# Kernel optimization log

Hardware: AMD Instinct MI355X
Metric: run time of the kernel (lower is better)

Reference implementation:

```python
import jax, jax.numpy as jnp
import numpy as np

B, T0, T, N, C, MS, K, I = 8, 12, 10, 3000, 64, 3, 3, 1
W = T - (MS - 1)           # 8 sliding windows / stack_gcn layers
K2 = MS + (MS - 1) * I     # conv2 kernel width = 5
DN = ('NCHW', 'OIHW', 'NCHW')


def setup_inputs() -> dict:
    key = jax.random.key(0)
    ks = jax.random.split(key, 11)
    s = 0.05
    return {
        'original_data': jax.random.normal(ks[0], (B, T0, N, C), jnp.float32),
        'data': jax.random.normal(ks[1], (B, T, N, C), jnp.float32),
        'adj_st': jax.random.uniform(ks[2], (N, MS * N), jnp.float32) * 0.01,
        'conv1_w': jax.random.normal(ks[3], (2 * C, C, 1, MS), jnp.float32) * s,
        'conv1_b': jax.random.normal(ks[4], (2 * C,), jnp.float32) * s,
        'conv2_w': jax.random.normal(ks[5], (2 * C, C, 1, K2), jnp.float32) * s,
        'conv2_b': jax.random.normal(ks[6], (2 * C,), jnp.float32) * s,
        'temb': jax.random.normal(ks[7], (1, T, 1, C), jnp.float32) * 0.0003,
        'semb': jax.random.normal(ks[8], (1, 1, N, C), jnp.float32) * 0.0003,
        'glu_w': jax.random.normal(ks[9], (W, K, C, 2 * C), jnp.float32) * s,
        'glu_b': jax.random.normal(ks[10], (W, K, 2 * C), jnp.float32) * s,
    }


def _gated_conv(x, w, b):
    # x: (B, T, N, C) -> NCHW (B, C, N, T), VALID conv over time axis
    t = jnp.transpose(x, (0, 3, 2, 1))
    t = jax.lax.conv_general_dilated(t, w, (1, 1), 'VALID', dimension_numbers=DN)
    t = t + b[None, :, None, None]
    lhs, rhs = jnp.split(t, 2, axis=1)
    return jax.nn.sigmoid(lhs) * rhs  # (B, C, N, T')


def reference(original_data, data, adj_st, conv1_w, conv1_b, conv2_w, conv2_b,
              temb, semb, glu_w, glu_b):
    # temporal gated convs (conv1 on data, conv2 on original_data; current_step != 12)
    dta = _gated_conv(data, conv1_w, conv1_b) + _gated_conv(original_data, conv2_w, conv2_b)
    data_res = jnp.transpose(dta, (0, 3, 2, 1))          # (B, W, N, C)

    # position embedding (add)
    x = data + temb + semb                               # (B, T, N, C)

    # all W sliding windows of length MS, batched over the window axis
    windows = jnp.stack([x[:, i:i + MS] for i in range(W)], axis=0)   # (W, B, MS, N, C)
    windows = jnp.transpose(windows.reshape(W, B, MS * N, C), (0, 2, 1, 3))  # (W, MS*N, B, C)

    wing = windows[:, :(MS - 1) * N]                     # (W, 2N, B, C) fixed context
    d = windows[:, -N:]                                  # (W, N, B, C)
    res = d

    outs = []
    for k in range(K):  # sequential GCN kernels (data dependency)
        cat = jnp.concatenate([wing, d], axis=1)         # (W, MS*N, B, C)
        y = jnp.einsum('nm,wmbc->wnbc', adj_st, cat)     # graph aggregation
        z = jnp.einsum('wnbc,wcd->wnbd', y, glu_w[:, k]) + glu_b[:, k][:, None, None, :]
        lhs, rhs = jnp.split(z, 2, axis=-1)
        d = lhs * jax.nn.sigmoid(rhs)                    # GLU
        outs.append(d)

    agg = jnp.max(jnp.stack(outs, axis=0), axis=0) + res  # (W, N, B, C)
    return jnp.transpose(agg, (2, 0, 1, 3)) + data_res    # (B, W, N, C)
```

## Files before the change

### kernel.cpp

```cpp
#include <hip/hip_runtime.h>
#include <hip/hip_bf16.h>
#include <math.h>

#define NN 3000
#define NP 3072
#define KA 3008
#define KB 9024
#define MY 3072
#define BD 8
#define TD 10
#define T0D 12
#define WD 8
#define TSLAB (512L*KA)
#define YSLAB (512L*MY)
#define MSLAB (512L*KA)

typedef __attribute__((ext_vector_type(8))) short short8;
typedef __attribute__((ext_vector_type(4))) float floatx4;

__device__ __forceinline__ float sigm(float x) { return 1.0f / (1.0f + __expf(-x)); }
__device__ __forceinline__ ushort f2b(float f) {
    __hip_bfloat16 h = __float2bfloat16(f);
    return *reinterpret_cast<ushort*>(&h);
}
__device__ __forceinline__ void ld_lds16(const void* g, void* l) {
    __builtin_amdgcn_global_load_lds((const __attribute__((address_space(1))) unsigned int*)g,
                                     (__attribute__((address_space(3))) unsigned int*)l, 16, 0, 0);
}

__global__ void prep_adj(const float* __restrict__ adj, ushort* __restrict__ adjb) {
    long i = (long)blockIdx.x * 256 + threadIdx.x;
    if (i >= 3072L * 2256) return;
    int r  = (int)(i / 2256);
    int c4 = (int)(i % 2256) * 4;
    ushort4 u = {0, 0, 0, 0};
    if (r < NN && c4 < 9000) {
        float4 v = *(const float4*)(adj + (long)r * 9000 + c4);
        u.x = f2b(v.x); u.y = f2b(v.y); u.z = f2b(v.z); u.w = f2b(v.w);
    }
    *(ushort4*)(adjb + (long)r * KB + c4) = u;
}

__global__ __launch_bounds__(256) void prep_xt(
    const float* __restrict__ data, const float* __restrict__ temb,
    const float* __restrict__ semb, ushort* __restrict__ xT2)
{
    const int t = blockIdx.z, b = blockIdx.y;
    const int m0 = blockIdx.x * 64;
    const int tid = threadIdx.x;
    const int tx = tid & 15, ty = tid >> 4;
    __shared__ float T[64][68];
    #pragma unroll
    for (int p = 0; p < 4; ++p) {
        int nl = p * 16 + ty;
        int n = m0 + nl;
        int c4 = tx * 4;
        float4 v = {0.f, 0.f, 0.f, 0.f};
        if (n < NN) {
            float4 dv = *(const float4*)(data + ((long)(b * TD + t) * NN + n) * 64 + c4);
            float4 tv = *(const float4*)(temb + t * 64 + c4);
            float4 sv = *(const float4*)(semb + n * 64 + c4);
            v.x = dv.x + tv.x + sv.x; v.y = dv.y + tv.y + sv.y;
            v.z = dv.z + tv.z + sv.z; v.w = dv.w + tv.w + sv.w;
        }
        T[c4 + 0][nl] = v.x; T[c4 + 1][nl] = v.y;
        T[c4 + 2][nl] = v.z; T[c4 + 3][nl] = v.w;
    }
    __syncthreads();
    #pragma unroll
    for (int p = 0; p < 4; ++p) {
        int c = p * 16 + ty;
        int m4 = tx * 4;
        ushort4 u;
        u.x = f2b(T[c][m4 + 0]); u.y = f2b(T[c][m4 + 1]);
        u.z = f2b(T[c][m4 + 2]); u.w = f2b(T[c][m4 + 3]);
        *(ushort4*)(xT2 + ((long)t * 512 + b * 64 + c) * KA + m0 + m4) = u;
    }
}

__global__ void prep_db(const float* __restrict__ src, ushort* __restrict__ dst, int Tt) {
    long i = (long)blockIdx.x * 256 + threadIdx.x;
    long tot = 8L * Tt * NP * 16;
    if (i >= tot) return;
    int c4 = (int)(i & 15) * 4;
    long r = i >> 4;
    int n = (int)(r % NP);
    long bt = r / NP;
    ushort4 u = {0, 0, 0, 0};
    if (n < NN) {
        float4 v = *(const float4*)(src + (bt * NN + n) * 64 + c4);
        u.x = f2b(v.x); u.y = f2b(v.y); u.z = f2b(v.z); u.w = f2b(v.w);
    }
    *(ushort4*)(dst + r * 64 + c4) = u;
}

__global__ void prep_wb(const float* __restrict__ c1w, const float* __restrict__ c2w,
                        ushort* __restrict__ wb) {
    int i = blockIdx.x * 256 + threadIdx.x;
    if (i >= 128 * 512) return;
    int r = i >> 9, k = i & 511;
    int q = r >> 6, jp = r & 63;
    int o = (jp < 32) ? (q * 32 + jp) : (64 + q * 32 + (jp - 32));
    int s = k >> 6, c = k & 63;
    float v = (s < 3) ? c1w[(o * 64 + c) * 3 + s] : c2w[(o * 64 + c) * 5 + (s - 3)];
    wb[i] = f2b(v);
}

__device__ __forceinline__ void issue_stage(
    const ushort*& gA, const ushort*& gB, int& stg,
    const ushort* aA1, const ushort* aB1,
    ushort* dA, ushort* dB, int wOff)
{
    ld_lds16(gA,           dA + wOff);
    ld_lds16(gA + 64 * KA, dA + 2048 + wOff);
    ld_lds16(gB,           dB + wOff);
    ld_lds16(gB + 64 * KB, dB + 2048 + wOff);
    ++stg;
    if (stg == 94) { gA = aA1; gB = aB1; }
    else           { gA += 32; gB += 32; }
}

__device__ __forceinline__ void gemm_body(
    const ushort* __restrict__ A0, const ushort* __restrict__ A1, int nseg,
    const ushort* __restrict__ Badj, int colOff0, int colOff1,
    float* __restrict__ Yp)
{
    const int m0 = blockIdx.x * 128;
    const int j0 = blockIdx.y * 128;
    const int tid = threadIdx.x;
    const int lane = tid & 63;
    const int wv = tid >> 6;
    __shared__ ushort shA[3][4096];
    __shared__ ushort shB[3][4096];
    floatx4 acc[4][4] = {};
    const int srow = wv * 16 + (lane >> 2);
    const int kswz = ((lane & 3) ^ ((lane >> 3) & 3)) * 8;
    const int wj = (wv >> 1) * 64, wm = (wv & 1) * 64;
    const int half = lane >> 4;
    const int rsub = lane & 15;
    const int hsw  = (half ^ ((rsub >> 1) & 3)) * 8;
    const int wOff = wv * 512;
    const int nkt = 94 * nseg;

    int offA[4], offB[4];
    #pragma unroll
    for (int i = 0; i < 4; ++i) {
        offA[i] = (wj + i * 16 + rsub) * 32 + hsw;
        offB[i] = (wm + i * 16 + rsub) * 32 + hsw;
    }

    const ushort* aA1 = A1 + (long)(j0 + srow) * KA + kswz;
    const ushort* aB1 = Badj + colOff1 + (long)(m0 + srow) * KB + kswz;
    const ushort* gA  = A0 + (long)(j0 + srow) * KA + kswz;
    const ushort* gB  = Badj + colOff0 + (long)(m0 + srow) * KB + kswz;
    int stg = 0;

    ushort *pA0 = shA[0], *pA1 = shA[1], *pA2 = shA[2];
    ushort *pB0 = shB[0], *pB1 = shB[1], *pB2 = shB[2];

    issue_stage(gA, gB, stg, aA1, aB1, pA0, pB0, wOff);
    issue_stage(gA, gB, stg, aA1, aB1, pA1, pB1, wOff);
    asm volatile("s_waitcnt vmcnt(4)" ::: "memory");
    __builtin_amdgcn_s_barrier();
    __builtin_amdgcn_sched_barrier(0);

    for (int s = 0; s < nkt; ++s) {
        if (s + 2 < nkt)
            issue_stage(gA, gB, stg, aA1, aB1, pA2, pB2, wOff);
        short8 af[4], bf[4];
        #pragma unroll
        for (int i = 0; i < 4; ++i)
            af[i] = *(const short8*)(pA0 + offA[i]);
        #pragma unroll
        for (int i = 0; i < 4; ++i)
            bf[i] = *(const short8*)(pB0 + offB[i]);
        #pragma unroll
        for (int i = 0; i < 4; ++i)
            #pragma unroll
            for (int jj = 0; jj < 4; ++jj)
                acc[i][jj] = __builtin_amdgcn_mfma_f32_16x16x32_bf16(af[i], bf[jj], acc[i][jj], 0, 0, 0);
        if (s + 2 < nkt) {
            asm volatile("s_waitcnt vmcnt(4)" ::: "memory");
        } else if (s + 1 < nkt) {
            asm volatile("s_waitcnt vmcnt(0)" ::: "memory");
        }
        __builtin_amdgcn_s_barrier();
        __builtin_amdgcn_sched_barrier(0);
        ushort* t;
        t = pA0; pA0 = pA1; pA1 = pA2; pA2 = t;
        t = pB0; pB0 = pB1; pB1 = pB2; pB2 = t;
    }

    #pragma unroll
    for (int i = 0; i < 4; ++i) {
        int jrow = j0 + wj + i * 16 + half * 4;
        #pragma unroll
        for (int jj = 0; jj < 4; ++jj) {
            int mcol = m0 + wm + jj * 16 + rsub;
            float* o = Yp + (long)jrow * MY + mcol;
            o[0L * MY] = acc[i][jj].x;
            o[1L * MY] = acc[i][jj].y;
            o[2L * MY] = acc[i][jj].z;
            o[3L * MY] = acc[i][jj].w;
        }
    }
}

__global__ __launch_bounds__(256) void gemm_mfma(
    const ushort* __restrict__ A0, const ushort* __restrict__ A1, int nseg, long aW,
    const ushort* __restrict__ Badj, int colOff0, int colOff1,
    float* __restrict__ Y)
{
    const int w = blockIdx.z;
    gemm_body(A0 + (long)w * aW, A1 + (long)w * aW, nseg,
              Badj, colOff0, colOff1, Y + (long)w * YSLAB);
}

__global__ __launch_bounds__(256) void gemm_wing_d0(
    const ushort* __restrict__ xT2, const ushort* __restrict__ Badj,
    float* __restrict__ ywing, float* __restrict__ yd)
{
    const int zz = blockIdx.z;
    if (zz < 8) {
        gemm_body(xT2 + (long)zz * TSLAB, xT2 + (long)(zz + 1) * TSLAB, 2,
                  Badj, 0, 3000, ywing + (long)zz * YSLAB);
    } else {
        const int w = zz - 8;
        const ushort* a = xT2 + (long)(w + 2) * TSLAB;
        gemm_body(a, a, 1, Badj, 6000, 0, yd + (long)w * YSLAB);
    }
}

__global__ __launch_bounds__(256) void conv_mfma(
    const ushort* __restrict__ datab, const ushort* __restrict__ origb,
    const ushort* __restrict__ wb,
    const float* __restrict__ b1, const float* __restrict__ b2,
    float* __restrict__ out)
{
    const int b = blockIdx.y >> 3, wt = blockIdx.y & 7;
    const int n0 = blockIdx.x * 128;
    const int tid = threadIdx.x;
    const int lane = tid & 63;
    const int wv = tid >> 6;
    __shared__ ushort lA[128 * 32];
    __shared__ ushort lB[128 * 32];
    floatx4 acc1[4][4] = {};
    floatx4 acc2[4][4] = {};
    const int srow = wv * 16 + (lane >> 2);
    const int kp8  = (lane & 3) * 8;
    const int wj = (wv >> 1) * 64, wm = (wv & 1) * 64;
    const int half = lane >> 4;
    const int rsub = lane & 15;
    #pragma unroll
    for (int kt = 0; kt < 16; ++kt) {
        const int k0 = kt * 32;
        const int s = k0 >> 6;
        const int koff = k0 & 63;
        const ushort* Ab = (s < 3) ? datab + (long)(b * TD + wt + s) * NP * 64
                                   : origb + (long)(b * T0D + wt + (s - 3)) * NP * 64;
        #pragma unroll
        for (int p = 0; p < 2; ++p) {
            const ushort* g = Ab + (long)(n0 + p * 64 + srow) * 64 + koff + kp8;
            ld_lds16(g, lA + p * 2048 + wv * 512);
        }
        #pragma unroll
        for (int p = 0; p < 2; ++p) {
            const ushort* g = wb + (long)(p * 64 + srow) * 512 + k0 + kp8;
            ld_lds16(g, lB + p * 2048 + wv * 512);
        }
        __syncthreads();
        short8 af[4], bf[4];
        #pragma unroll
        for (int i = 0; i < 4; ++i)
            af[i] = *(const short8*)(lA + (wj + i * 16 + rsub) * 32 + half * 8);
        #pragma unroll
        for (int i = 0; i < 4; ++i)
            bf[i] = *(const short8*)(lB + (wm + i * 16 + rsub) * 32 + half * 8);
        if (kt < 6) {
            #pragma unroll
            for (int i = 0; i < 4; ++i)
                #pragma unroll
                for (int jj = 0; jj < 4; ++jj)
                    acc1[i][jj] = __builtin_amdgcn_mfma_f32_16x16x32_bf16(af[i], bf[jj], acc1[i][jj], 0, 0, 0);
        } else {
            #pragma unroll
            for (int i = 0; i < 4; ++i)
                #pragma unroll
                for (int jj = 0; jj < 4; ++jj)
                    acc2[i][jj] = __builtin_amdgcn_mfma_f32_16x16x32_bf16(af[i], bf[jj], acc2[i][jj], 0, 0, 0);
        }
        __syncthreads();
    }
    const int q = wv & 1;
    float* outp = out + (long)(b * WD + wt) * NN * 64;
    #pragma unroll
    for (int i = 0; i < 4; ++i) {
        const int nbase = n0 + wj + i * 16 + half * 4;
        #pragma unroll
        for (int jj = 0; jj < 2; ++jj) {
            const int ol = q * 32 + jj * 16 + rsub;
            const float bl1 = b1[ol], br1 = b1[64 + ol];
            const float bl2 = b2[ol], br2 = b2[64 + ol];
            float zl1[4] = {acc1[i][jj].x, acc1[i][jj].y, acc1[i][jj].z, acc1[i][jj].w};
            float zr1[4] = {acc1[i][jj+2].x, acc1[i][jj+2].y, acc1[i][jj+2].z, acc1[i][jj+2].w};
            float zl2[4] = {acc2[i][jj].x, acc2[i][jj].y, acc2[i][jj].z, acc2[i][jj].w};
            float zr2[4] = {acc2[i][jj+2].x, acc2[i][jj+2].y, acc2[i][jj+2].z, acc2[i][jj+2].w};
            #pragma unroll
            for (int r = 0; r < 4; ++r) {
                int n = nbase + r;
                if (n < NN) {
                    float ov = sigm(zl1[r] + bl1) * (zr1[r] + br1)
                             + sigm(zl2[r] + bl2) * (zr2[r] + br2);
                    outp[(long)n * 64 + ol] = ov;
                }
            }
        }
    }
}

__global__ __launch_bounds__(256) void glu_t(
    const float* __restrict__ Yd, const float* __restrict__ Ywing,
    const float* __restrict__ gw_all, const float* __restrict__ gb_all,
    int kIdx, ushort* __restrict__ dp, float* __restrict__ maxd)
{
    const int w = blockIdx.y;
    const int m0 = blockIdx.x * 64;
    const int tid = threadIdx.x;
    const int tx = tid & 15, ty = tid >> 4;
    const float* Ydp = Yd + (long)w * YSLAB;
    const float* Ywp = Ywing + (long)w * YSLAB;
    ushort* dpp = dp + (long)w * TSLAB;
    float* mdp = maxd + (long)w * MSLAB;
    const float* gw = gw_all + (long)(w * 3 + kIdx) * 8192;
    const float* gb = gb_all + (w * 3 + kIdx) * 128;
    __shared__ float gws[64][132];
    __shared__ float Ys[64][68];
    #pragma unroll
    for (int p = 0; p < 8; ++p) {
        int r = p * 8 + (tid >> 5);
        int c0 = (tid & 31) * 4;
        *(float4*)&gws[r][c0] = *(const float4*)(gw + r * 128 + c0);
    }
    for (int b = 0; b < 8; ++b) {
        if (b) __syncthreads();
        #pragma unroll
        for (int p = 0; p < 4; ++p) {
            int c = p * 16 + ty;
            long off = (long)(b * 64 + c) * MY + m0 + tx * 4;
            float4 v1 = *(const float4*)(Ydp + off);
            float4 v2 = *(const float4*)(Ywp + off);
            Ys[c][tx * 4 + 0] = v1.x + v2.x;
            Ys[c][tx * 4 + 1] = v1.y + v2.y;
            Ys[c][tx * 4 + 2] = v1.z + v2.z;
            Ys[c][tx * 4 + 3] = v1.w + v2.w;
        }
        __syncthreads();
        float acc[8][4] = {{0.f}};
        for (int c = 0; c < 64; ++c) {
            float4 ym = *(const float4*)&Ys[c][tx * 4];
            #pragma unroll
            for (int p = 0; p < 8; ++p) {
                float a = gws[c][ty + p * 16];
                acc[p][0] = fmaf(a, ym.x, acc[p][0]);
                acc[p][1] = fmaf(a, ym.y, acc[p][1]);
                acc[p][2] = fmaf(a, ym.z, acc[p][2]);
                acc[p][3] = fmaf(a, ym.w, acc[p][3]);
            }
        }
        #pragma unroll
        for (int p = 0; p < 4; ++p) {
            int c = ty + p * 16;
            float bl = gb[c], br = gb[64 + c];
            long row = (long)(b * 64 + c) * KA + m0 + tx * 4;
            float d[4];
            #pragma unroll
            for (int q = 0; q < 4; ++q) {
                float zl = acc[p][q] + bl;
                float zr = acc[p + 4][q] + br;
                d[q] = zl * sigm(zr);
            }
            int mb = m0 + tx * 4;
            if (kIdx < 2) {
                ushort4 u;
                u.x = (mb + 0 < NN) ? f2b(d[0]) : (ushort)0;
                u.y = (mb + 1 < NN) ? f2b(d[1]) : (ushort)0;
                u.z = (mb + 2 < NN) ? f2b(d[2]) : (ushort)0;
                u.w = (mb + 3 < NN) ? f2b(d[3]) : (ushort)0;
                *(ushort4*)(dpp + row) = u;
            }
            if (kIdx == 0) {
                float4 m4 = {d[0], d[1], d[2], d[3]};
                *(float4*)(mdp + row) = m4;
            } else {
                float4 old = *(const float4*)(mdp + row);
                float4 m4;
                m4.x = fmaxf(old.x, d[0]); m4.y = fmaxf(old.y, d[1]);
                m4.z = fmaxf(old.z, d[2]); m4.w = fmaxf(old.w, d[3]);
                *(float4*)(mdp + row) = m4;
            }
        }
    }
}

__global__ __launch_bounds__(256) void final_t(
    const float* __restrict__ maxd, const float* __restrict__ data,
    const float* __restrict__ temb, const float* __restrict__ semb,
    float* __restrict__ out)
{
    const int w = blockIdx.z, b = blockIdx.y;
    const int m0 = blockIdx.x * 64;
    const int tid = threadIdx.x;
    const int tx = tid & 15, ty = tid >> 4;
    const float* mdp = maxd + (long)w * MSLAB;
    __shared__ float T[64][68];
    #pragma unroll
    for (int p = 0; p < 4; ++p) {
        int c = p * 16 + ty;
        float4 v = *(const float4*)(mdp + (long)(b * 64 + c) * KA + m0 + tx * 4);
        T[c][tx * 4 + 0] = v.x; T[c][tx * 4 + 1] = v.y;
        T[c][tx * 4 + 2] = v.z; T[c][tx * 4 + 3] = v.w;
    }
    __syncthreads();
    #pragma unroll
    for (int p = 0; p < 4; ++p) {
        int nl = p * 16 + ty;
        int n = m0 + nl;
        if (n < NN) {
            int c4 = tx * 4;
            long oidx = ((long)(b * WD + w) * NN + n) * 64 + c4;
            float4 o  = *(const float4*)(out + oidx);
            float4 dd = *(const float4*)(data + ((long)(b * TD + w + 2) * NN + n) * 64 + c4);
            float4 tv = *(const float4*)(temb + (w + 2) * 64 + c4);
            float4 sv = *(const float4*)(semb + n * 64 + c4);
            o.x += T[c4 + 0][nl] + dd.x + tv.x + sv.x;
            o.y += T[c4 + 1][nl] + dd.y + tv.y + sv.y;
            o.z += T[c4 + 2][nl] + dd.z + tv.z + sv.z;
            o.w += T[c4 + 3][nl] + dd.w + tv.w + sv.w;
            *(float4*)(out + oidx) = o;
        }
    }
}

extern "C" void kernel_launch(void* const* d_in, const int* in_sizes, int n_in,
                              void* d_out, int out_size, void* d_ws, size_t ws_size,
                              hipStream_t stream) {
    const float* orig = (const float*)d_in[0];
    const float* data = (const float*)d_in[1];
    const float* adj  = (const float*)d_in[2];
    const float* c1w  = (const float*)d_in[3];
    const float* c1b  = (const float*)d_in[4];
    const float* c2w  = (const float*)d_in[5];
    const float* c2b  = (const float*)d_in[6];
    const float* temb = (const float*)d_in[7];
    const float* semb = (const float*)d_in[8];
    const float* gw   = (const float*)d_in[9];
    const float* gb   = (const float*)d_in[10];
    float* out = (float*)d_out;

    char* ws = (char*)d_ws;
    ushort* adjb = (ushort*)ws;                          ws += 3072L * 9024 * 2;
    ushort* xT2  = (ushort*)ws;                          ws += 10L * TSLAB * 2;
    ushort* dpb  = (ushort*)ws;                          ws += 8L * TSLAB * 2;
    float*  ywing = (float*)ws;                          ws += 8L * YSLAB * 4;
    float*  yd    = (float*)ws;                          ws += 8L * YSLAB * 4;
    float*  maxd  = (float*)ws;

    ushort* wb    = (ushort*)ywing;
    ushort* datab = (ushort*)yd;
    ushort* origb = (ushort*)maxd;

    prep_adj<<<dim3(27072), 256, 0, stream>>>(adj, adjb);
    prep_xt<<<dim3(47, 8, 10), 256, 0, stream>>>(data, temb, semb, xT2);
    prep_db<<<dim3(15360), 256, 0, stream>>>(data, datab, TD);
    prep_db<<<dim3(18432), 256, 0, stream>>>(orig, origb, T0D);
    prep_wb<<<dim3(256), 256, 0, stream>>>(c1w, c2w, wb);

    conv_mfma<<<dim3(24, 64), 256, 0, stream>>>(datab, origb, wb, c1b, c2b, out);

    gemm_wing_d0<<<dim3(24, 4, 16), 256, 0, stream>>>(xT2, adjb, ywing, yd);
    glu_t<<<dim3(47, 8), 256, 0, stream>>>(yd, ywing, gw, gb, 0, dpb, maxd);
    gemm_mfma<<<dim3(24, 4, 8), 256, 0, stream>>>(dpb, dpb, 1, TSLAB, adjb, 6000, 0, yd);
    glu_t<<<dim3(47, 8), 256, 0, stream>>>(yd, ywing, gw, gb, 1, dpb, maxd);
    gemm_mfma<<<dim3(24, 4, 8), 256, 0, stream>>>(dpb, dpb, 1, TSLAB, adjb, 6000, 0, yd);
    glu_t<<<dim3(47, 8), 256, 0, stream>>>(yd, ywing, gw, gb, 2, dpb, maxd);

    final_t<<<dim3(47, 8, 8), 256, 0, stream>>>(maxd, data, temb, semb, out);
}
```

Baseline: 1.126 ms.

## Fuse prep kernels, triple-buffer conv LDS loads, parallelize GLU over batch

Merges the five preprocessing kernels into one launch that dispatches on block index, which removes per-launch overhead. The conv_mfma loop now uses a three-stage LDS ring with XOR-swizzled offsets and vmcnt-based waits, so global-to-LDS loads overlap MFMA work and LDS bank conflicts drop. glu_t moves its batch loop into a grid dimension, giving eight times more blocks to fill the GPU. The costs are higher LDS use in the conv kernel, which may lower occupancy, and hand-written waitcnt and swizzle logic that has to match the load order exactly.

```diff
diff --git a/kernel.cpp b/kernel.cpp
--- a/kernel.cpp
+++ b/kernel.cpp
@@ -28,82 +28,92 @@
                                      (__attribute__((address_space(3))) unsigned int*)l, 16, 0, 0);
 }
 
-__global__ void prep_adj(const float* __restrict__ adj, ushort* __restrict__ adjb) {
-    long i = (long)blockIdx.x * 256 + threadIdx.x;
-    if (i >= 3072L * 2256) return;
-    int r  = (int)(i / 2256);
-    int c4 = (int)(i % 2256) * 4;
-    ushort4 u = {0, 0, 0, 0};
-    if (r < NN && c4 < 9000) {
-        float4 v = *(const float4*)(adj + (long)r * 9000 + c4);
-        u.x = f2b(v.x); u.y = f2b(v.y); u.z = f2b(v.z); u.w = f2b(v.w);
-    }
-    *(ushort4*)(adjb + (long)r * KB + c4) = u;
-}
-
-__global__ __launch_bounds__(256) void prep_xt(
-    const float* __restrict__ data, const float* __restrict__ temb,
-    const float* __restrict__ semb, ushort* __restrict__ xT2)
-{
-    const int t = blockIdx.z, b = blockIdx.y;
-    const int m0 = blockIdx.x * 64;
+__global__ __launch_bounds__(256) void prep_all(
+    const float* __restrict__ adj, const float* __restrict__ data,
+    const float* __restrict__ orig, const float* __restrict__ temb,
+    const float* __restrict__ semb, const float* __restrict__ c1w,
+    const float* __restrict__ c2w,
+    ushort* __restrict__ adjb, ushort* __restrict__ xT2,
+    ushort* __restrict__ datab, ushort* __restrict__ origb,
+    ushort* __restrict__ wb)
+{
+    const int blk = blockIdx.x;
     const int tid = threadIdx.x;
-    const int tx = tid & 15, ty = tid >> 4;
     __shared__ float T[64][68];
-    #pragma unroll
-    for (int p = 0; p < 4; ++p) {
-        int nl = p * 16 + ty;
-        int n = m0 + nl;
-        int c4 = tx * 4;
-        float4 v = {0.f, 0.f, 0.f, 0.f};
+
+    if (blk < 27072) {
+        long i = (long)blk * 256 + tid;
+        if (i >= 3072L * 2256) return;
+        int r  = (int)(i / 2256);
+        int c4 = (int)(i % 2256) * 4;
+        ushort4 u = {0, 0, 0, 0};
+        if (r < NN && c4 < 9000) {
+            float4 v = *(const float4*)(adj + (long)r * 9000 + c4);
+            u.x = f2b(v.x); u.y = f2b(v.y); u.z = f2b(v.z); u.w = f2b(v.w);
+        }
+        *(ushort4*)(adjb + (long)r * KB + c4) = u;
+    } else if (blk < 30832) {
+        int id = blk - 27072;
+        const int x = id % 47;  id /= 47;
+        const int b = id & 7;
+        const int t = id >> 3;
+        const int m0 = x * 64;
+        const int tx = tid & 15, ty = tid >> 4;
+        #pragma unroll
+        for (int p = 0; p < 4; ++p) {
+            int nl = p * 16 + ty;
+            int n = m0 + nl;
+            int c4 = tx * 4;
+            float4 v = {0.f, 0.f, 0.f, 0.f};
+            if (n < NN) {
+                float4 dv = *(const float4*)(data + ((long)(b * TD + t) * NN + n) * 64 + c4);
+                float4 tv = *(const float4*)(temb + t * 64 + c4);
+                float4 sv = *(const float4*)(semb + n * 64 + c4);
+                v.x = dv.x + tv.x + sv.x; v.y = dv.y + tv.y + sv.y;
+                v.z = dv.z + tv.z + sv.z; v.w = dv.w + tv.w + sv.w;
+            }
+            T[c4 + 0][nl] = v.x; T[c4 + 1][nl] = v.y;
+            T[c4 + 2][nl] = v.z; T[c4 + 3][nl] = v.w;
+        }
+        __syncthreads();
+        #pragma unroll
+        for (int p = 0; p < 4; ++p) {
+            int c = p * 16 + ty;
+            int m4 = tx * 4;
+            ushort4 u;
+            u.x = f2b(T[c][m4 + 0]); u.y = f2b(T[c][m4 + 1]);
+            u.z = f2b(T[c][m4 + 2]); u.w = f2b(T[c][m4 + 3]);
+            *(ushort4*)(xT2 + ((long)t * 512 + b * 64 + c) * KA + m0 + m4) = u;
+        }
+    } else if (blk < 64624) {
+        const int isData = (blk < 46192);
+        const int base = isData ? 30832 : 46192;
+        const int Tt = isData ? TD : T0D;
+        const float* src = isData ? data : orig;
+        ushort* dst = isData ? datab : origb;
+        long i = (long)(blk - base) * 256 + tid;
+        long tot = 8L * Tt * NP * 16;
+        if (i >= tot) return;
+        int c4 = (int)(i & 15) * 4;
+        long r = i >> 4;
+        int n = (int)(r % NP);
+        long bt = r / NP;
+        ushort4 u = {0, 0, 0, 0};
         if (n < NN) {
-            float4 dv = *(const float4*)(data + ((long)(b * TD + t) * NN + n) * 64 + c4);
-            float4 tv = *(const float4*)(temb + t * 64 + c4);
-            float4 sv = *(const float4*)(semb + n * 64 + c4);
-            v.x = dv.x + tv.x + sv.x; v.y = dv.y + tv.y + sv.y;
-            v.z = dv.z + tv.z + sv.z; v.w = dv.w + tv.w + sv.w;
-        }
-        T[c4 + 0][nl] = v.x; T[c4 + 1][nl] = v.y;
-        T[c4 + 2][nl] = v.z; T[c4 + 3][nl] = v.w;
-    }
-    __syncthreads();
-    #pragma unroll
-    for (int p = 0; p < 4; ++p) {
-        int c = p * 16 + ty;
-        int m4 = tx * 4;
-        ushort4 u;
-        u.x = f2b(T[c][m4 + 0]); u.y = f2b(T[c][m4 + 1]);
-        u.z = f2b(T[c][m4 + 2]); u.w = f2b(T[c][m4 + 3]);
-        *(ushort4*)(xT2 + ((long)t * 512 + b * 64 + c) * KA + m0 + m4) = u;
-    }
-}
-
-__global__ void prep_db(const float* __restrict__ src, ushort* __restrict__ dst, int Tt) {
-    long i = (long)blockIdx.x * 256 + threadIdx.x;
-    long tot = 8L * Tt * NP * 16;
-    if (i >= tot) return;
-    int c4 = (int)(i & 15) * 4;
-    long r = i >> 4;
-    int n = (int)(r % NP);
-    long bt = r / NP;
-    ushort4 u = {0, 0, 0, 0};
-    if (n < NN) {
-        float4 v = *(const float4*)(src + (bt * NN + n) * 64 + c4);
-        u.x = f2b(v.x); u.y = f2b(v.y); u.z = f2b(v.z); u.w = f2b(v.w);
-    }
-    *(ushort4*)(dst + r * 64 + c4) = u;
-}
-
-__global__ void prep_wb(const float* __restrict__ c1w, const float* __restrict__ c2w,
-                        ushort* __restrict__ wb) {
-    int i = blockIdx.x * 256 + threadIdx.x;
-    if (i >= 128 * 512) return;
-    int r = i >> 9, k = i & 511;
-    int q = r >> 6, jp = r & 63;
-    int o = (jp < 32) ? (q * 32 + jp) : (64 + q * 32 + (jp - 32));
-    int s = k >> 6, c = k & 63;
-    float v = (s < 3) ? c1w[(o * 64 + c) * 3 + s] : c2w[(o * 64 + c) * 5 + (s - 3)];
-    wb[i] = f2b(v);
+            float4 v = *(const float4*)(src + (bt * NN + n) * 64 + c4);
+            u.x = f2b(v.x); u.y = f2b(v.y); u.z = f2b(v.z); u.w = f2b(v.w);
+        }
+        *(ushort4*)(dst + r * 64 + c4) = u;
+    } else {
+        int i = (blk - 64624) * 256 + tid;
+        if (i >= 128 * 512) return;
+        int r = i >> 9, k = i & 511;
+        int q = r >> 6, jp = r & 63;
+        int o = (jp < 32) ? (q * 32 + jp) : (64 + q * 32 + (jp - 32));
+        int s = k >> 6, c = k & 63;
+        float v = (s < 3) ? c1w[(o * 64 + c) * 3 + s] : c2w[(o * 64 + c) * 5 + (s - 3)];
+        wb[i] = f2b(v);
+    }
 }
 
 __device__ __forceinline__ void issue_stage(
@@ -242,41 +252,57 @@
     const int tid = threadIdx.x;
     const int lane = tid & 63;
     const int wv = tid >> 6;
-    __shared__ ushort lA[128 * 32];
-    __shared__ ushort lB[128 * 32];
+    __shared__ ushort shA[3][4096];
+    __shared__ ushort shB[3][4096];
     floatx4 acc1[4][4] = {};
     floatx4 acc2[4][4] = {};
     const int srow = wv * 16 + (lane >> 2);
-    const int kp8  = (lane & 3) * 8;
+    const int kswz = ((lane & 3) ^ ((lane >> 3) & 3)) * 8;
     const int wj = (wv >> 1) * 64, wm = (wv & 1) * 64;
     const int half = lane >> 4;
     const int rsub = lane & 15;
-    #pragma unroll
-    for (int kt = 0; kt < 16; ++kt) {
-        const int k0 = kt * 32;
-        const int s = k0 >> 6;
-        const int koff = k0 & 63;
-        const ushort* Ab = (s < 3) ? datab + (long)(b * TD + wt + s) * NP * 64
-                                   : origb + (long)(b * T0D + wt + (s - 3)) * NP * 64;
-        #pragma unroll
-        for (int p = 0; p < 2; ++p) {
-            const ushort* g = Ab + (long)(n0 + p * 64 + srow) * 64 + koff + kp8;
-            ld_lds16(g, lA + p * 2048 + wv * 512);
-        }
-        #pragma unroll
-        for (int p = 0; p < 2; ++p) {
-            const ushort* g = wb + (long)(p * 64 + srow) * 512 + k0 + kp8;
-            ld_lds16(g, lB + p * 2048 + wv * 512);
-        }
-        __syncthreads();
+    const int hsw  = (half ^ ((rsub >> 1) & 3)) * 8;
+    const int wOff = wv * 512;
+
+    int offA[4], offB[4];
+    #pragma unroll
+    for (int i = 0; i < 4; ++i) {
+        offA[i] = (wj + i * 16 + rsub) * 32 + hsw;
+        offB[i] = (wm + i * 16 + rsub) * 32 + hsw;
+    }
+
+    auto stage = [&](int kt, ushort* dA, ushort* dB) {
+        const int sl = kt >> 1, koff = (kt & 1) * 32;
+        const ushort* Ab = (sl < 3) ? datab + (long)(b * TD + wt + sl) * NP * 64
+                                    : origb + (long)(b * T0D + wt + (sl - 3)) * NP * 64;
+        const ushort* gA = Ab + (long)(n0 + srow) * 64 + koff + kswz;
+        ld_lds16(gA,           dA + wOff);
+        ld_lds16(gA + 64 * 64, dA + 2048 + wOff);
+        const ushort* gB = wb + (long)srow * 512 + kt * 32 + kswz;
+        ld_lds16(gB,            dB + wOff);
+        ld_lds16(gB + 64 * 512, dB + 2048 + wOff);
+    };
+
+    ushort *pA0 = shA[0], *pA1 = shA[1], *pA2 = shA[2];
+    ushort *pB0 = shB[0], *pB1 = shB[1], *pB2 = shB[2];
+
+    stage(0, pA0, pB0);
+    stage(1, pA1, pB1);
+    asm volatile("s_waitcnt vmcnt(4)" ::: "memory");
+    __builtin_amdgcn_s_barrier();
+    __builtin_amdgcn_sched_barrier(0);
+
+    for (int s = 0; s < 16; ++s) {
+        if (s + 2 < 16)
+            stage(s + 2, pA2, pB2);
         short8 af[4], bf[4];
         #pragma unroll
         for (int i = 0; i < 4; ++i)
-            af[i] = *(const short8*)(lA + (wj + i * 16 + rsub) * 32 + half * 8);
+            af[i] = *(const short8*)(pA0 + offA[i]);
         #pragma unroll
         for (int i = 0; i < 4; ++i)
-            bf[i] = *(const short8*)(lB + (wm + i * 16 + rsub) * 32 + half * 8);
-        if (kt < 6) {
+            bf[i] = *(const short8*)(pB0 + offB[i]);
+        if (s < 6) {
             #pragma unroll
             for (int i = 0; i < 4; ++i)
                 #pragma unroll
@@ -289,8 +315,18 @@
                 for (int jj = 0; jj < 4; ++jj)
                     acc2[i][jj] = __builtin_amdgcn_mfma_f32_16x16x32_bf16(af[i], bf[jj], acc2[i][jj], 0, 0, 0);
         }
-        __syncthreads();
-    }
+        if (s + 2 < 16) {
+            asm volatile("s_waitcnt vmcnt(4)" ::: "memory");
+        } else if (s + 1 < 16) {
+            asm volatile("s_waitcnt vmcnt(0)" ::: "memory");
+        }
+        __builtin_amdgcn_s_barrier();
+        __builtin_amdgcn_sched_barrier(0);
+        ushort* t;
+        t = pA0; pA0 = pA1; pA1 = pA2; pA2 = t;
+        t = pB0; pB0 = pB1; pB1 = pB2; pB2 = t;
+    }
+
     const int q = wv & 1;
     float* outp = out + (long)(b * WD + wt) * NN * 64;
     #pragma unroll
@@ -324,6 +360,7 @@
     int kIdx, ushort* __restrict__ dp, float* __restrict__ maxd)
 {
     const int w = blockIdx.y;
+    const int b = blockIdx.z;
     const int m0 = blockIdx.x * 64;
     const int tid = threadIdx.x;
     const int tx = tid & 15, ty = tid >> 4;
@@ -341,63 +378,60 @@
         int c0 = (tid & 31) * 4;
         *(float4*)&gws[r][c0] = *(const float4*)(gw + r * 128 + c0);
     }
-    for (int b = 0; b < 8; ++b) {
-        if (b) __syncthreads();
-        #pragma unroll
-        for (int p = 0; p < 4; ++p) {
-            int c = p * 16 + ty;
-            long off = (long)(b * 64 + c) * MY + m0 + tx * 4;
-            float4 v1 = *(const float4*)(Ydp + off);
-            float4 v2 = *(const float4*)(Ywp + off);
-            Ys[c][tx * 4 + 0] = v1.x + v2.x;
-            Ys[c][tx * 4 + 1] = v1.y + v2.y;
-            Ys[c][tx * 4 + 2] = v1.z + v2.z;
-            Ys[c][tx * 4 + 3] = v1.w + v2.w;
-        }
-        __syncthreads();
-        float acc[8][4] = {{0.f}};
-        for (int c = 0; c < 64; ++c) {
-            float4 ym = *(const float4*)&Ys[c][tx * 4];
-            #pragma unroll
-            for (int p = 0; p < 8; ++p) {
-                float a = gws[c][ty + p * 16];
-                acc[p][0] = fmaf(a, ym.x, acc[p][0]);
-                acc[p][1] = fmaf(a, ym.y, acc[p][1]);
-                acc[p][2] = fmaf(a, ym.z, acc[p][2]);
-                acc[p][3] = fmaf(a, ym.w, acc[p][3]);
-            }
-        }
-        #pragma unroll
-        for (int p = 0; p < 4; ++p) {
-            int c = ty + p * 16;
-            float bl = gb[c], br = gb[64 + c];
-            long row = (long)(b * 64 + c) * KA + m0 + tx * 4;
-            float d[4];
-            #pragma unroll
-            for (int q = 0; q < 4; ++q) {
-                float zl = acc[p][q] + bl;
-                float zr = acc[p + 4][q] + br;
-                d[q] = zl * sigm(zr);
-            }
-            int mb = m0 + tx * 4;
-            if (kIdx < 2) {
-                ushort4 u;
-                u.x = (mb + 0 < NN) ? f2b(d[0]) : (ushort)0;
-                u.y = (mb + 1 < NN) ? f2b(d[1]) : (ushort)0;
-                u.z = (mb + 2 < NN) ? f2b(d[2]) : (ushort)0;
-                u.w = (mb + 3 < NN) ? f2b(d[3]) : (ushort)0;
-                *(ushort4*)(dpp + row) = u;
-            }
-            if (kIdx == 0) {
-                float4 m4 = {d[0], d[1], d[2], d[3]};
-                *(float4*)(mdp + row) = m4;
-            } else {
-                float4 old = *(const float4*)(mdp + row);
-                float4 m4;
-                m4.x = fmaxf(old.x, d[0]); m4.y = fmaxf(old.y, d[1]);
-                m4.z = fmaxf(old.z, d[2]); m4.w = fmaxf(old.w, d[3]);
-                *(float4*)(mdp + row) = m4;
-            }
+    #pragma unroll
+    for (int p = 0; p < 4; ++p) {
+        int c = p * 16 + ty;
+        long off = (long)(b * 64 + c) * MY + m0 + tx * 4;
+        float4 v1 = *(const float4*)(Ydp + off);
+        float4 v2 = *(const float4*)(Ywp + off);
+        Ys[c][tx * 4 + 0] = v1.x + v2.x;
+        Ys[c][tx * 4 + 1] = v1.y + v2.y;
+        Ys[c][tx * 4 + 2] = v1.z + v2.z;
+        Ys[c][tx * 4 + 3] = v1.w + v2.w;
+    }
+    __syncthreads();
+    float acc[8][4] = {{0.f}};
+    for (int c = 0; c < 64; ++c) {
+        float4 ym = *(const float4*)&Ys[c][tx * 4];
+        #pragma unroll
+        for (int p = 0; p < 8; ++p) {
+            float a = gws[c][ty + p * 16];
+            acc[p][0] = fmaf(a, ym.x, acc[p][0]);
+            acc[p][1] = fmaf(a, ym.y, acc[p][1]);
+            acc[p][2] = fmaf(a, ym.z, acc[p][2]);
+            acc[p][3] = fmaf(a, ym.w, acc[p][3]);
+        }
+    }
+    #pragma unroll
+    for (int p = 0; p < 4; ++p) {
+        int c = ty + p * 16;
+        float bl = gb[c], br = gb[64 + c];
+        long row = (long)(b * 64 + c) * KA + m0 + tx * 4;
+        float d[4];
+        #pragma unroll
+        for (int q = 0; q < 4; ++q) {
+            float zl = acc[p][q] + bl;
+            float zr = acc[p + 4][q] + br;
+            d[q] = zl * sigm(zr);
+        }
+        int mb = m0 + tx * 4;
+        if (kIdx < 2) {
+            ushort4 u;
+            u.x = (mb + 0 < NN) ? f2b(d[0]) : (ushort)0;
+            u.y = (mb + 1 < NN) ? f2b(d[1]) : (ushort)0;
+            u.z = (mb + 2 < NN) ? f2b(d[2]) : (ushort)0;
+            u.w = (mb + 3 < NN) ? f2b(d[3]) : (ushort)0;
+            *(ushort4*)(dpp + row) = u;
+        }
+        if (kIdx == 0) {
+            float4 m4 = {d[0], d[1], d[2], d[3]};
+            *(float4*)(mdp + row) = m4;
+        } else {
+            float4 old = *(const float4*)(mdp + row);
+            float4 m4;
+            m4.x = fmaxf(old.x, d[0]); m4.y = fmaxf(old.y, d[1]);
+            m4.z = fmaxf(old.z, d[2]); m4.w = fmaxf(old.w, d[3]);
+            *(float4*)(mdp + row) = m4;
         }
     }
 }
@@ -469,20 +503,17 @@
     ushort* datab = (ushort*)yd;
     ushort* origb = (ushort*)maxd;
 
-    prep_adj<<<dim3(27072), 256, 0, stream>>>(adj, adjb);
-    prep_xt<<<dim3(47, 8, 10), 256, 0, stream>>>(data, temb, semb, xT2);
-    prep_db<<<dim3(15360), 256, 0, stream>>>(data, datab, TD);
-    prep_db<<<dim3(18432), 256, 0, stream>>>(orig, origb, T0D);
-    prep_wb<<<dim3(256), 256, 0, stream>>>(c1w, c2w, wb);
+    prep_all<<<dim3(64880), 256, 0, stream>>>(adj, data, orig, temb, semb, c1w, c2w,
+                                              adjb, xT2, datab, origb, wb);
 
     conv_mfma<<<dim3(24, 64), 256, 0, stream>>>(datab, origb, wb, c1b, c2b, out);
 
     gemm_wing_d0<<<dim3(24, 4, 16), 256, 0, stream>>>(xT2, adjb, ywing, yd);
-    glu_t<<<dim3(47, 8), 256, 0, stream>>>(yd, ywing, gw, gb, 0, dpb, maxd);
+    glu_t<<<dim3(47, 8, 8), 256, 0, stream>>>(yd, ywing, gw, gb, 0, dpb, maxd);
     gemm_mfma<<<dim3(24, 4, 8), 256, 0, stream>>>(dpb, dpb, 1, TSLAB, adjb, 6000, 0, yd);
-    glu_t<<<dim3(47, 8), 256, 0, stream>>>(yd, ywing, gw, gb, 1, dpb, maxd);
+    glu_t<<<dim3(47, 8, 8), 256, 0, stream>>>(yd, ywing, gw, gb, 1, dpb, maxd);
     gemm_mfma<<<dim3(24, 4, 8), 256, 0, stream>>>(dpb, dpb, 1, TSLAB, adjb, 6000, 0, yd);
-    glu_t<<<dim3(47, 8), 256, 0, stream>>>(yd, ywing, gw, gb, 2, dpb, maxd);
+    glu_t<<<dim3(47, 8, 8), 256, 0, stream>>>(yd, ywing, gw, gb, 2, dpb, maxd);
 
     final_t<<<dim3(47, 8, 8), 256, 0, stream>>>(maxd, data, temb, semb, out);
 }
```

Result: slower. 1.153 ms (+2.4%).
